# Kernel optimization log

Measured on AMD Instinct MI355X. Metric: run time of the kernel, lower is better.

Reference implementation:

```python
import jax, jax.numpy as jnp
import numpy as np

NUM_CAMS, B, C, H, W = 6, 2, 64, 232, 400
N = 200000  # number of sparse voxels across the batch


def setup_inputs() -> dict:
    key = jax.random.key(0)
    k1, k2, k3, k4, k5, k6 = jax.random.split(key, 6)
    return {
        "img_feats": jax.random.normal(k1, (NUM_CAMS, B, C, H, W), dtype=jnp.float32),
        "voxel_feats": jax.random.normal(k2, (N, C), dtype=jnp.float32),
        "voxel_batch_idx": jax.random.randint(k3, (N,), 0, B, dtype=jnp.int32),
        "grid_y": jax.random.randint(k4, (NUM_CAMS, N), 0, H, dtype=jnp.int32),
        "grid_x": jax.random.randint(k5, (NUM_CAMS, N), 0, W, dtype=jnp.int32),
        "point_mask": jax.random.randint(k6, (NUM_CAMS, N), 0, 2, dtype=jnp.int32),
    }


def reference(img_feats, voxel_feats, voxel_batch_idx, grid_y, grid_x, point_mask):
    # For each camera: fuse_feat = image_feat[:, grid_y, grid_x] gathered from the
    # per-sample feature map selected by voxel_batch_idx; then (sum fuse mode)
    # voxel_feat[mask] += fuse_feat. Cameras accumulate sequentially, which for
    # 'sum' is equivalent to summing masked contributions over cameras.
    def gather_cam(feat_bchw, gy, gx):
        # feat_bchw: (B, C, H, W); gy, gx: (N,) -> (N, C)
        return feat_bchw[voxel_batch_idx, :, gy, gx]

    fuse = jax.vmap(gather_cam)(img_feats, grid_y, grid_x)  # (NUM_CAMS, N, C)
    mask = (point_mask > 0).astype(voxel_feats.dtype)        # (NUM_CAMS, N)
    return voxel_feats + jnp.einsum("knc,kn->nc", fuse, mask)
```

## Files before the change

### kernel.cpp

```cpp
#include <hip/hip_runtime.h>
#include <hip/hip_fp16.h>

#define NUM_CAMS 6
#define B_DIM    2
#define C_DIM    64
#define H_DIM    232
#define W_DIM    400
#define HW_DIM   (H_DIM * W_DIM)
#define TILES_PER_PLANE (HW_DIM / 64)
#define PLANES   (NUM_CAMS * B_DIM)

typedef float  f4  __attribute__((ext_vector_type(4)));
typedef unsigned int u32;

__global__ __launch_bounds__(256) void transpose_f16_kernel(
    const float* __restrict__ img,
    __half*      __restrict__ wsp)
{
    __shared__ float tile[64][65];

    const int t   = blockIdx.x;
    const int kb  = blockIdx.y;
    const int px0 = t * 64;
    const size_t plane_in  = (size_t)kb * C_DIM * HW_DIM;
    const size_t plane_out = (size_t)kb * HW_DIM * C_DIM;
    const int tid = threadIdx.x;

    {
        const int pq = tid & 15;
        const int cg = tid >> 4;
#pragma unroll
        for (int r = 0; r < 4; ++r) {
            const int c = r * 16 + cg;
            const f4 v = __builtin_nontemporal_load(
                (const f4*)&img[plane_in + (size_t)c * HW_DIM + px0 + pq * 4]);
            tile[c][pq * 4 + 0] = v.x;
            tile[c][pq * 4 + 1] = v.y;
            tile[c][pq * 4 + 2] = v.z;
            tile[c][pq * 4 + 3] = v.w;
        }
    }
    __syncthreads();
    {
        const int c2 = (tid & 31) * 2;
        const int pg = tid >> 5;
#pragma unroll
        for (int r = 0; r < 8; ++r) {
            const int p = r * 8 + pg;
            const __half2 h = __floats2half2_rn(tile[c2][p], tile[c2 + 1][p]);
            *(__half2*)&wsp[plane_out + (size_t)(px0 + p) * C_DIM + c2] = h;
        }
    }
}

__global__ __launch_bounds__(256) void fuse_f16_kernel(
    const __half* __restrict__ wsp,
    const float*  __restrict__ vox,
    const int*    __restrict__ bidx,
    const int*    __restrict__ gy,
    const int*    __restrict__ gx,
    const int*    __restrict__ mask,
    float*        __restrict__ out,
    int N)
{
    const size_t gt = blockIdx.x * (size_t)blockDim.x + threadIdx.x;
    const int n = (int)(gt >> 4);
    const int q = (int)(gt & 15);
    if (n >= N) return;

    int m[NUM_CAMS], y[NUM_CAMS], x[NUM_CAMS];
#pragma unroll
    for (int k = 0; k < NUM_CAMS; ++k) {
        m[k] = mask[(size_t)k * N + n];
        y[k] = gy[(size_t)k * N + n];
        x[k] = gx[(size_t)k * N + n];
    }
    const int b = bidx[n];

    f4 acc = __builtin_nontemporal_load((const f4*)vox + (size_t)n * 16 + q);

    const __half* base = wsp + (size_t)b * HW_DIM * C_DIM;

    uint2 rv[NUM_CAMS];
#pragma unroll
    for (int k = 0; k < NUM_CAMS; ++k) {
        rv[k] = make_uint2(0u, 0u);
        if (m[k] > 0) {
            const __half* p = base
                + (size_t)k * ((size_t)B_DIM * HW_DIM * C_DIM)
                + ((size_t)y[k] * W_DIM + x[k]) * C_DIM;
            rv[k] = *(const uint2*)(p + q * 4);
        }
    }

#pragma unroll
    for (int k = 0; k < NUM_CAMS; ++k) {
        const __half2 a = *(const __half2*)&rv[k].x;
        const __half2 c = *(const __half2*)&rv[k].y;
        const float2 fa = __half22float2(a);
        const float2 fc = __half22float2(c);
        acc.x += fa.x; acc.y += fa.y; acc.z += fc.x; acc.w += fc.y;
    }

    __builtin_nontemporal_store(acc, (f4*)out + (size_t)n * 16 + q);
}

__global__ __launch_bounds__(256) void fuse_direct_kernel(
    const float* __restrict__ img, const float* __restrict__ vox,
    const int* __restrict__ bidx, const int* __restrict__ gy,
    const int* __restrict__ gx, const int* __restrict__ mask,
    float* __restrict__ out, int N)
{
    const int wave = (int)((blockIdx.x * (size_t)blockDim.x + threadIdx.x) >> 6);
    const int c    = threadIdx.x & 63;
    if (wave >= N) return;
    const int n = wave;
    int m[NUM_CAMS], y[NUM_CAMS], x[NUM_CAMS];
#pragma unroll
    for (int k = 0; k < NUM_CAMS; ++k) {
        m[k] = mask[(size_t)k * N + n];
        y[k] = gy[(size_t)k * N + n];
        x[k] = gx[(size_t)k * N + n];
    }
    const int b = bidx[n];
    float acc = vox[(size_t)n * C_DIM + c];
    const float* base = img + ((size_t)b * C_DIM + c) * HW_DIM;
    float v[NUM_CAMS];
#pragma unroll
    for (int k = 0; k < NUM_CAMS; ++k) {
        v[k] = 0.0f;
        if (m[k] > 0)
            v[k] = base[(size_t)k * (B_DIM * C_DIM * (size_t)HW_DIM)
                        + (size_t)y[k] * W_DIM + (size_t)x[k]];
    }
    acc += ((v[0] + v[1]) + (v[2] + v[3])) + (v[4] + v[5]);
    out[(size_t)n * C_DIM + c] = acc;
}

extern "C" void kernel_launch(void* const* d_in, const int* in_sizes, int n_in,
                              void* d_out, int out_size, void* d_ws, size_t ws_size,
                              hipStream_t stream) {
    const float* img  = (const float*)d_in[0];
    const float* vox  = (const float*)d_in[1];
    const int*   bidx = (const int*)d_in[2];
    const int*   gy   = (const int*)d_in[3];
    const int*   gx   = (const int*)d_in[4];
    const int*   mask = (const int*)d_in[5];
    float* out = (float*)d_out;

    const int N = in_sizes[2];

    const size_t img_half_bytes = (size_t)PLANES * HW_DIM * C_DIM * sizeof(__half);

    if (ws_size >= img_half_bytes) {
        __half* wsp = (__half*)d_ws;
        dim3 tgrid(TILES_PER_PLANE, PLANES);
        transpose_f16_kernel<<<tgrid, 256, 0, stream>>>(img, wsp);

        const size_t total_threads = (size_t)N * 16;
        const int blocks = (int)((total_threads + 255) / 256);
        fuse_f16_kernel<<<blocks, 256, 0, stream>>>(wsp, vox, bidx, gy, gx, mask, out, N);
    } else {
        const int blocks = (N * 64 + 255) / 256;
        fuse_direct_kernel<<<blocks, 256, 0, stream>>>(img, vox, bidx, gy, gx, mask, out, N);
    }
}
```

Before: 106.8 us.

## Skip fp16 transpose writes for pixels no voxel samples, using occupancy flags

Adds two kernels that zero a per-plane byte flag map and mark every pixel referenced by a masked voxel for each camera and batch. The transpose kernel then writes the fp16 channel-last copy only for flagged pixels, which cuts write traffic to the workspace. It still reads the whole image, though, and the expected coverage is about 600k samples over roughly 1.1M pixels, so many pixels are still written. The change costs two extra launches and the flag memset and scatter. It also needs a larger workspace, and falls back to the old path when the workspace is too small.

```diff
diff --git a/kernel.cpp b/kernel.cpp
--- a/kernel.cpp
+++ b/kernel.cpp
@@ -10,12 +10,35 @@
 #define TILES_PER_PLANE (HW_DIM / 64)
 #define PLANES   (NUM_CAMS * B_DIM)
 
-typedef float  f4  __attribute__((ext_vector_type(4)));
+typedef float f4 __attribute__((ext_vector_type(4)));
 typedef unsigned int u32;
+typedef unsigned char u8;
+
+__global__ __launch_bounds__(256) void zero_flags_kernel(u32* __restrict__ f, int n32)
+{
+    const int t = blockIdx.x * 256 + threadIdx.x;
+    if (t < n32) f[t] = 0u;
+}
+
+__global__ __launch_bounds__(256) void flag_kernel(
+    const int* __restrict__ bidx, const int* __restrict__ gy,
+    const int* __restrict__ gx, const int* __restrict__ mask,
+    u8* __restrict__ flags, int N)
+{
+    const int n = blockIdx.x * 256 + threadIdx.x;
+    const int k = blockIdx.y;
+    if (n >= N) return;
+    if (mask[(size_t)k * N + n] > 0) {
+        const int plane = k * B_DIM + bidx[n];
+        const int pix = gy[(size_t)k * N + n] * W_DIM + gx[(size_t)k * N + n];
+        flags[(size_t)plane * HW_DIM + pix] = 1;
+    }
+}
 
 __global__ __launch_bounds__(256) void transpose_f16_kernel(
     const float* __restrict__ img,
-    __half*      __restrict__ wsp)
+    __half*      __restrict__ wsp,
+    const u8*    __restrict__ flags)
 {
     __shared__ float tile[64][65];
 
@@ -47,8 +70,11 @@
 #pragma unroll
         for (int r = 0; r < 8; ++r) {
             const int p = r * 8 + pg;
-            const __half2 h = __floats2half2_rn(tile[c2][p], tile[c2 + 1][p]);
-            *(__half2*)&wsp[plane_out + (size_t)(px0 + p) * C_DIM + c2] = h;
+            const bool wr = (flags == nullptr) || (flags[(size_t)kb * HW_DIM + px0 + p] != 0);
+            if (wr) {
+                const __half2 h = __floats2half2_rn(tile[c2][p], tile[c2 + 1][p]);
+                *(__half2*)&wsp[plane_out + (size_t)(px0 + p) * C_DIM + c2] = h;
+            }
         }
     }
 }
@@ -150,16 +176,28 @@
 
     const int N = in_sizes[2];
 
-    const size_t img_half_bytes = (size_t)PLANES * HW_DIM * C_DIM * sizeof(__half);
-
-    if (ws_size >= img_half_bytes) {
+    const size_t wsp_bytes   = (size_t)PLANES * HW_DIM * C_DIM * sizeof(__half);
+    const size_t flags_off   = (wsp_bytes + 255) & ~(size_t)255;
+    const size_t flags_bytes = (size_t)PLANES * HW_DIM;
+    const size_t need_flags  = flags_off + flags_bytes;
+
+    dim3 tgrid(TILES_PER_PLANE, PLANES);
+    dim3 mgrid((N + 255) / 256, NUM_CAMS);
+    const int fuse_blocks = (int)(((size_t)N * 16 + 255) / 256);
+
+    if (ws_size >= need_flags) {
         __half* wsp = (__half*)d_ws;
-        dim3 tgrid(TILES_PER_PLANE, PLANES);
-        transpose_f16_kernel<<<tgrid, 256, 0, stream>>>(img, wsp);
-
-        const size_t total_threads = (size_t)N * 16;
-        const int blocks = (int)((total_threads + 255) / 256);
-        fuse_f16_kernel<<<blocks, 256, 0, stream>>>(wsp, vox, bidx, gy, gx, mask, out, N);
+        u8* flags = (u8*)d_ws + flags_off;
+
+        const int n32 = (int)(flags_bytes / 4);
+        zero_flags_kernel<<<(n32 + 255) / 256, 256, 0, stream>>>((u32*)flags, n32);
+        flag_kernel<<<mgrid, 256, 0, stream>>>(bidx, gy, gx, mask, flags, N);
+        transpose_f16_kernel<<<tgrid, 256, 0, stream>>>(img, wsp, flags);
+        fuse_f16_kernel<<<fuse_blocks, 256, 0, stream>>>(wsp, vox, bidx, gy, gx, mask, out, N);
+    } else if (ws_size >= wsp_bytes) {
+        __half* wsp = (__half*)d_ws;
+        transpose_f16_kernel<<<tgrid, 256, 0, stream>>>(img, wsp, nullptr);
+        fuse_f16_kernel<<<fuse_blocks, 256, 0, stream>>>(wsp, vox, bidx, gy, gx, mask, out, N);
     } else {
         const int blocks = (N * 64 + 255) / 256;
         fuse_direct_kernel<<<blocks, 256, 0, stream>>>(img, vox, bidx, gy, gx, mask, out, N);
```

Result: slower. 117.9 us (+10.4%).

## Stage voxel indices in shared memory and process four voxels per thread

Applied to the files above, without the earlier changes.

The fuse kernel now loads mask, grid coordinates and batch indices for 64 voxels into shared memory once per block with coalesced loads, instead of having all 16 lanes per voxel redundantly load the same scalars. Each thread then handles four voxels, issuing up to 24 independent gathers for more memory-level parallelism. The cost is more registers per thread, a block barrier, and four times fewer blocks, which may reduce occupancy.

```diff
diff --git a/kernel.cpp b/kernel.cpp
--- a/kernel.cpp
+++ b/kernel.cpp
@@ -9,9 +9,10 @@
 #define HW_DIM   (H_DIM * W_DIM)
 #define TILES_PER_PLANE (HW_DIM / 64)
 #define PLANES   (NUM_CAMS * B_DIM)
+#define VPB      64
+#define ILP      4
 
-typedef float  f4  __attribute__((ext_vector_type(4)));
-typedef unsigned int u32;
+typedef float f4 __attribute__((ext_vector_type(4)));
 
 __global__ __launch_bounds__(256) void transpose_f16_kernel(
     const float* __restrict__ img,
@@ -53,7 +54,7 @@
     }
 }
 
-__global__ __launch_bounds__(256) void fuse_f16_kernel(
+__global__ __launch_bounds__(256) void fuse_f16x4_kernel(
     const __half* __restrict__ wsp,
     const float*  __restrict__ vox,
     const int*    __restrict__ bidx,
@@ -63,46 +64,75 @@
     float*        __restrict__ out,
     int N)
 {
-    const size_t gt = blockIdx.x * (size_t)blockDim.x + threadIdx.x;
-    const int n = (int)(gt >> 4);
-    const int q = (int)(gt & 15);
-    if (n >= N) return;
+    __shared__ int sm[NUM_CAMS][VPB];
+    __shared__ int sy[NUM_CAMS][VPB];
+    __shared__ int sx[NUM_CAMS][VPB];
+    __shared__ int sb[VPB];
 
-    int m[NUM_CAMS], y[NUM_CAMS], x[NUM_CAMS];
+    const int v0  = blockIdx.x * VPB;
+    const int tid = threadIdx.x;
+
+    {
+        const int jj = tid & 63;
+        const int v  = v0 + jj;
+        const int vc = (v < N) ? v : (N - 1);
+        for (int r = tid >> 6; r < 19; r += 4) {
+            if (r < 6) {
+                sm[r][jj] = (v < N) ? mask[(size_t)r * N + vc] : 0;
+            } else if (r < 12) {
+                sy[r - 6][jj] = gy[(size_t)(r - 6) * N + vc];
+            } else if (r < 18) {
+                sx[r - 12][jj] = gx[(size_t)(r - 12) * N + vc];
+            } else {
+                sb[jj] = bidx[vc];
+            }
+        }
+    }
+    __syncthreads();
+
+    const int j = tid >> 4;
+    const int q = tid & 15;
+
+    f4 acc[ILP];
+    uint2 rv[ILP][NUM_CAMS];
+    int vn[ILP];
+
 #pragma unroll
-    for (int k = 0; k < NUM_CAMS; ++k) {
-        m[k] = mask[(size_t)k * N + n];
-        y[k] = gy[(size_t)k * N + n];
-        x[k] = gx[(size_t)k * N + n];
+    for (int ii = 0; ii < ILP; ++ii) {
+        const int s = j + ii * 16;
+        const int v = v0 + s;
+        vn[ii] = v;
+        const int vc = (v < N) ? v : (N - 1);
+        acc[ii] = __builtin_nontemporal_load((const f4*)vox + (size_t)vc * 16 + q);
     }
-    const int b = bidx[n];
 
-    f4 acc = __builtin_nontemporal_load((const f4*)vox + (size_t)n * 16 + q);
-
-    const __half* base = wsp + (size_t)b * HW_DIM * C_DIM;
-
-    uint2 rv[NUM_CAMS];
 #pragma unroll
-    for (int k = 0; k < NUM_CAMS; ++k) {
-        rv[k] = make_uint2(0u, 0u);
-        if (m[k] > 0) {
-            const __half* p = base
-                + (size_t)k * ((size_t)B_DIM * HW_DIM * C_DIM)
-                + ((size_t)y[k] * W_DIM + x[k]) * C_DIM;
-            rv[k] = *(const uint2*)(p + q * 4);
+    for (int ii = 0; ii < ILP; ++ii) {
+        const int s = j + ii * 16;
+        const __half* base = wsp + (size_t)sb[s] * HW_DIM * C_DIM;
+#pragma unroll
+        for (int k = 0; k < NUM_CAMS; ++k) {
+            rv[ii][k] = make_uint2(0u, 0u);
+            if (sm[k][s] > 0) {
+                const __half* p = base
+                    + (size_t)k * ((size_t)B_DIM * HW_DIM * C_DIM)
+                    + ((size_t)sy[k][s] * W_DIM + sx[k][s]) * C_DIM;
+                rv[ii][k] = *(const uint2*)(p + q * 4);
+            }
         }
     }
 
 #pragma unroll
-    for (int k = 0; k < NUM_CAMS; ++k) {
-        const __half2 a = *(const __half2*)&rv[k].x;
-        const __half2 c = *(const __half2*)&rv[k].y;
-        const float2 fa = __half22float2(a);
-        const float2 fc = __half22float2(c);
-        acc.x += fa.x; acc.y += fa.y; acc.z += fc.x; acc.w += fc.y;
+    for (int ii = 0; ii < ILP; ++ii) {
+#pragma unroll
+        for (int k = 0; k < NUM_CAMS; ++k) {
+            const float2 fa = __half22float2(*(const __half2*)&rv[ii][k].x);
+            const float2 fc = __half22float2(*(const __half2*)&rv[ii][k].y);
+            acc[ii].x += fa.x; acc[ii].y += fa.y; acc[ii].z += fc.x; acc[ii].w += fc.y;
+        }
+        if (vn[ii] < N)
+            __builtin_nontemporal_store(acc[ii], (f4*)out + (size_t)vn[ii] * 16 + q);
     }
-
-    __builtin_nontemporal_store(acc, (f4*)out + (size_t)n * 16 + q);
 }
 
 __global__ __launch_bounds__(256) void fuse_direct_kernel(
@@ -157,9 +187,8 @@
         dim3 tgrid(TILES_PER_PLANE, PLANES);
         transpose_f16_kernel<<<tgrid, 256, 0, stream>>>(img, wsp);
 
-        const size_t total_threads = (size_t)N * 16;
-        const int blocks = (int)((total_threads + 255) / 256);
-        fuse_f16_kernel<<<blocks, 256, 0, stream>>>(wsp, vox, bidx, gy, gx, mask, out, N);
+        const int blocks = (N + VPB - 1) / VPB;
+        fuse_f16x4_kernel<<<blocks, 256, 0, stream>>>(wsp, vox, bidx, gy, gx, mask, out, N);
     } else {
         const int blocks = (N * 64 + 255) / 256;
         fuse_direct_kernel<<<blocks, 256, 0, stream>>>(img, vox, bidx, gy, gx, mask, out, N);
```

Result: faster. 103.4 us (-3.2%).
